# Optimization experiments

Measured on AMD Instinct MI355X. Metric: run time of the kernel, lower is better.

## Reference

```python
import jax, jax.numpy as jnp
import numpy as np

N, M_CTX, SIN, YDIM, SPROJ = 16384, 4096, 256, 7, 256


def setup_inputs() -> dict:
    key = jax.random.key(0)
    k1, k2, k3, k4, k5 = jax.random.split(key, 5)
    return {
        "x": jax.random.normal(k1, (N, SIN), dtype=jnp.float32),
        "y": jax.random.normal(k2, (M_CTX, YDIM), dtype=jnp.float32),
        "Wq": jax.random.normal(k3, (SIN, SPROJ), dtype=jnp.float32) / np.sqrt(SIN),
        "Wk": jax.random.normal(k4, (YDIM, SPROJ), dtype=jnp.float32) / np.sqrt(YDIM),
        "Wv": jax.random.normal(k5, (YDIM, SPROJ), dtype=jnp.float32) / np.sqrt(YDIM),
    }


def smooth_softmax(x):
    # softmax over keys (axis=1) blended with 0.1*relu, renormalized
    s = jax.nn.softmax(x, axis=1)
    num = jax.nn.relu(x) * 0.1 + s
    return num / jnp.sum(num, axis=1, keepdims=True)


def reference(x, y, Wq, Wk, Wv):
    XQ = x @ Wq            # [N, P]
    YK = y @ Wk            # [M, P]
    YV = y @ Wv            # [M, P]
    scores = (XQ @ YK.T) / jnp.sqrt(jnp.asarray(YK.shape[1], XQ.dtype))  # [N, M]
    A = smooth_softmax(scores)
    return A @ YV          # [N, P]
```

## Files before the change

kernel.cpp:

```cpp
#include <hip/hip_runtime.h>
#include <hip/hip_bf16.h>

#define N_Q   16384
#define MCTX  4096
#define DSIN  256
#define YDIM  7
#define PDIM  256
#define BK    32

typedef __attribute__((ext_vector_type(8))) short s16x8;
typedef __attribute__((ext_vector_type(4))) float f32x4;
typedef unsigned short u16;

static __device__ __forceinline__ u16 f2bf(float f) {
    union { float f; unsigned u; } v; v.f = f;
    unsigned r = v.u + 0x7fffu + ((v.u >> 16) & 1u);
    return (u16)(r >> 16);
}
static __device__ __forceinline__ float bf2f(u16 h) {
    union { unsigned u; float f; } v; v.u = ((unsigned)h) << 16;
    return v.f;
}
static __device__ __forceinline__ f32x4 mfma16(s16x8 a, s16x8 b, f32x4 c) {
    return __builtin_amdgcn_mfma_f32_16x16x32_bf16(a, b, c, 0, 0, 0);
}
static __device__ __forceinline__ void gload_lds16(const u16* g, u16* l) {
    __builtin_amdgcn_global_load_lds(
        (const __attribute__((address_space(1))) unsigned int*)(g),
        (__attribute__((address_space(3))) unsigned int*)(l), 16, 0, 0);
}

__global__ void k_wt(const float* __restrict__ Wq, u16* __restrict__ WtH,
                     u16* __restrict__ WtL) {
    int n = blockIdx.x;
    int k = threadIdx.x;
    float w = Wq[(size_t)k * PDIM + n];
    u16 h = f2bf(w);
    WtH[(size_t)n * DSIN + k] = h;
    WtL[(size_t)n * DSIN + k] = f2bf(w - bf2f(h));
}

__global__ void k_ykv(const float* __restrict__ y, const float* __restrict__ Wk,
                      const float* __restrict__ Wv, u16* __restrict__ YK,
                      u16* __restrict__ YVb) {
    int kb = blockIdx.x;
    int p  = threadIdx.x;
    float wk[YDIM], wv[YDIM];
#pragma unroll
    for (int j = 0; j < YDIM; ++j) {
        wk[j] = Wk[(size_t)j * PDIM + p];
        wv[j] = Wv[(size_t)j * PDIM + p];
    }
    u16 vbuf[32];
#pragma unroll
    for (int m = 0; m < 32; ++m) {
        int key = kb * 32 + m;
        float ak = 0.f, av = 0.f;
#pragma unroll
        for (int j = 0; j < YDIM; ++j) {
            float yy = y[(size_t)key * YDIM + j];
            ak += yy * wk[j];
            av += yy * wv[j];
        }
        YK[(size_t)key * PDIM + p] = f2bf(ak * 0.0625f);
        vbuf[m] = f2bf(av);
    }
    s16x8* dst = (s16x8*)(YVb + ((size_t)kb * PDIM + p) * 32);
#pragma unroll
    for (int c = 0; c < 4; ++c) dst[c] = ((s16x8*)vbuf)[c];
}

__global__ __launch_bounds__(256, 1) void k_xq(const float* __restrict__ x,
                                               const u16* __restrict__ WtH,
                                               const u16* __restrict__ WtL,
                                               u16* __restrict__ XQ) {
    __shared__ u16 xH[64 * 256];
    __shared__ u16 xL[64 * 256];
    const int tid = threadIdx.x;
    const int rowg0 = blockIdx.x * 64;

#pragma unroll
    for (int i = 0; i < 8; ++i) {
        int row = (tid >> 5) + i * 8;
        int c32 = tid & 31;
        const float* px = x + (size_t)(rowg0 + row) * DSIN + c32 * 8;
        float4 a = *(const float4*)px;
        float4 b = *(const float4*)(px + 4);
        float vals[8] = {a.x, a.y, a.z, a.w, b.x, b.y, b.z, b.w};
        s16x8 h, l;
#pragma unroll
        for (int j = 0; j < 8; ++j) {
            u16 hh = f2bf(vals[j]);
            h[j] = (short)hh;
            l[j] = (short)f2bf(vals[j] - bf2f(hh));
        }
        int pc = c32 ^ (row & 7);
        *(s16x8*)(xH + row * 256 + pc * 8) = h;
        *(s16x8*)(xL + row * 256 + pc * 8) = l;
    }
    __syncthreads();

    const int wave = tid >> 6, lane = tid & 63;
    const int quad = lane >> 4, m16 = lane & 15;
    const int rowl = wave * 16 + m16;
    const int swz = rowl & 7;
    s16x8 ah[8], al[8];
#pragma unroll
    for (int kf = 0; kf < 8; ++kf) {
        int pc = (kf * 4 + quad) ^ swz;
        ah[kf] = *(const s16x8*)(xH + rowl * 256 + pc * 8);
        al[kf] = *(const s16x8*)(xL + rowl * 256 + pc * 8);
    }
#pragma unroll
    for (int pt = 0; pt < 16; ++pt) {
        f32x4 acc = (f32x4){0.f, 0.f, 0.f, 0.f};
#pragma unroll
        for (int kf = 0; kf < 8; ++kf) {
            size_t idx = (size_t)(pt * 16 + m16) * DSIN + kf * 32 + quad * 8;
            s16x8 bh = *(const s16x8*)(WtH + idx);
            s16x8 bl = *(const s16x8*)(WtL + idx);
            acc = mfma16(ah[kf], bh, acc);
            acc = mfma16(al[kf], bh, acc);
            acc = mfma16(ah[kf], bl, acc);
        }
#pragma unroll
        for (int r = 0; r < 4; ++r)
            XQ[(size_t)(rowg0 + wave * 16 + quad * 4 + r) * PDIM + pt * 16 + m16] =
                f2bf(acc[r]);
    }
}

__global__ __launch_bounds__(256, 2) void k_attn(const u16* __restrict__ XQ,
                                                 const u16* __restrict__ YK,
                                                 const u16* __restrict__ YVb,
                                                 float* __restrict__ accE,
                                                 float* __restrict__ accR,
                                                 float* __restrict__ lsum,
                                                 float* __restrict__ rsum,
                                                 int msPerSplit) {
    __shared__ u16 Kt[32 * 256];
    __shared__ u16 Pe[64 * 40];
    __shared__ u16 Pr[64 * 40];

    const int tid = threadIdx.x;
    const int wave = tid >> 6, lane = tid & 63;
    const int quad = lane >> 4, m16 = lane & 15;
    const int split = blockIdx.y;
    const int qbase = blockIdx.x * 64;
    const int key_begin = split * msPerSplit;
    const int iters = msPerSplit / BK;
    const int pslice = wave * 64;
    const int swz = m16 & 7;

    s16x8 qf[8];
    const u16* qp = XQ + (size_t)(qbase + wave * 16 + m16) * DSIN;
#pragma unroll
    for (int kf = 0; kf < 8; ++kf)
        qf[kf] = *(const s16x8*)(qp + kf * 32 + quad * 8);

    f32x4 aE[4][4], aR[4][4];
#pragma unroll
    for (int g = 0; g < 4; ++g)
#pragma unroll
        for (int t = 0; t < 4; ++t) {
            aE[g][t] = (f32x4){0.f, 0.f, 0.f, 0.f};
            aR[g][t] = (f32x4){0.f, 0.f, 0.f, 0.f};
        }
    float lacc[4] = {0.f, 0.f, 0.f, 0.f}, racc[4] = {0.f, 0.f, 0.f, 0.f};

    auto stage = [&](int key0) {
#pragma unroll
        for (int c = 0; c < 4; ++c) {
            int l = (wave * 4 + c) * 64 + lane;
            int r = l >> 5;
            int sc = (l & 31) ^ (r & 7);
            gload_lds16(YK + (size_t)(key0 + r) * DSIN + sc * 8,
                        Kt + (size_t)(wave * 4 + c) * 512);
        }
    };
    stage(key_begin);

    for (int it = 0; it < iters; ++it) {
        const int key0 = key_begin + it * BK;
        __syncthreads();

        f32x4 s0 = (f32x4){0.f, 0.f, 0.f, 0.f};
        f32x4 s1 = (f32x4){0.f, 0.f, 0.f, 0.f};
#pragma unroll
        for (int kf = 0; kf < 8; ++kf) {
            int pc = (kf * 4 + quad) ^ swz;
            s16x8 b0 = *(const s16x8*)(Kt + m16 * 256 + pc * 8);
            s16x8 b1 = *(const s16x8*)(Kt + (16 + m16) * 256 + pc * 8);
            s0 = mfma16(qf[kf], b0, s0);
            s1 = mfma16(qf[kf], b1, s1);
        }
#pragma unroll
        for (int r = 0; r < 4; ++r) {
            float e0 = __expf(s0[r]), e1 = __expf(s1[r]);
            float rl0 = fmaxf(s0[r], 0.f), rl1 = fmaxf(s1[r], 0.f);
            lacc[r] += e0 + e1;
            racc[r] += rl0 + rl1;
            int row = wave * 16 + quad * 4 + r;
            Pe[row * 40 + m16]      = f2bf(e0);
            Pe[row * 40 + 16 + m16] = f2bf(e1);
            Pr[row * 40 + m16]      = f2bf(rl0);
            Pr[row * 40 + 16 + m16] = f2bf(rl1);
        }
        __syncthreads();

        s16x8 vf[4];
        const u16* vb = YVb + (size_t)((key0 >> 5) * PDIM) * 32;
#pragma unroll
        for (int t = 0; t < 4; ++t)
            vf[t] = *(const s16x8*)(vb + (size_t)(pslice + t * 16 + m16) * 32 + quad * 8);

        if (it + 1 < iters) stage(key0 + BK);

#pragma unroll
        for (int g = 0; g < 4; ++g) {
            s16x8 pa = *(const s16x8*)(Pe + (g * 16 + m16) * 40 + quad * 8);
            s16x8 pb = *(const s16x8*)(Pr + (g * 16 + m16) * 40 + quad * 8);
#pragma unroll
            for (int t = 0; t < 4; ++t) {
                aE[g][t] = mfma16(pa, vf[t], aE[g][t]);
                aR[g][t] = mfma16(pb, vf[t], aR[g][t]);
            }
        }
    }

    size_t ob = ((size_t)split * N_Q + qbase) * PDIM;
#pragma unroll
    for (int g = 0; g < 4; ++g)
#pragma unroll
        for (int t = 0; t < 4; ++t)
#pragma unroll
            for (int r = 0; r < 4; ++r) {
                size_t o = ob + (size_t)(g * 16 + quad * 4 + r) * PDIM + pslice + t * 16 + m16;
                accE[o] = aE[g][t][r];
                accR[o] = aR[g][t][r];
            }
#pragma unroll
    for (int r = 0; r < 4; ++r) {
        lacc[r] += __shfl_xor(lacc[r], 1);
        lacc[r] += __shfl_xor(lacc[r], 2);
        lacc[r] += __shfl_xor(lacc[r], 4);
        lacc[r] += __shfl_xor(lacc[r], 8);
        racc[r] += __shfl_xor(racc[r], 1);
        racc[r] += __shfl_xor(racc[r], 2);
        racc[r] += __shfl_xor(racc[r], 4);
        racc[r] += __shfl_xor(racc[r], 8);
    }
    if (m16 < 4) {
        float lv = (m16 == 0) ? lacc[0] : (m16 == 1) ? lacc[1] : (m16 == 2) ? lacc[2] : lacc[3];
        float rv = (m16 == 0) ? racc[0] : (m16 == 1) ? racc[1] : (m16 == 2) ? racc[2] : racc[3];
        int row = split * N_Q + qbase + wave * 16 + quad * 4 + m16;
        lsum[row] = lv;
        rsum[row] = rv;
    }
}

__global__ void k_comb(const float* __restrict__ accE, const float* __restrict__ accR,
                       const float* __restrict__ lsum, const float* __restrict__ rsum,
                       float* __restrict__ out, int nsplit) {
    int row = blockIdx.x * 4 + (threadIdx.x >> 6);
    size_t idx = (size_t)row * PDIM + (threadIdx.x & 63) * 4;
    const size_t NP = (size_t)N_Q * PDIM;
    float4 E = {0.f, 0.f, 0.f, 0.f}, R = {0.f, 0.f, 0.f, 0.f};
    float L = 0.f, Rs = 0.f;
    for (int s = 0; s < nsplit; ++s) {
        float4 e = *(const float4*)(accE + s * NP + idx);
        float4 r = *(const float4*)(accR + s * NP + idx);
        E.x += e.x; E.y += e.y; E.z += e.z; E.w += e.w;
        R.x += r.x; R.y += r.y; R.z += r.z; R.w += r.w;
        L  += lsum[(size_t)s * N_Q + row];
        Rs += rsum[(size_t)s * N_Q + row];
    }
    float invL = 1.f / L, invD = 1.f / (1.f + 0.1f * Rs);
    float4 o;
    o.x = (0.1f * R.x + E.x * invL) * invD;
    o.y = (0.1f * R.y + E.y * invL) * invD;
    o.z = (0.1f * R.z + E.z * invL) * invD;
    o.w = (0.1f * R.w + E.w * invL) * invD;
    *(float4*)(out + idx) = o;
}

extern "C" void kernel_launch(void* const* d_in, const int* in_sizes, int n_in,
                              void* d_out, int out_size, void* d_ws, size_t ws_size,
                              hipStream_t stream) {
    const float* x  = (const float*)d_in[0];
    const float* y  = (const float*)d_in[1];
    const float* Wq = (const float*)d_in[2];
    const float* Wk = (const float*)d_in[3];
    const float* Wv = (const float*)d_in[4];
    float* out = (float*)d_out;

    char* ws = (char*)d_ws;
    size_t off = 0;
    auto take = [&](size_t bytes) -> char* {
        char* p = ws + off;
        off += (bytes + 255) & ~(size_t)255;
        return p;
    };
    u16* XQ  = (u16*)take((size_t)N_Q * PDIM * 2);
    u16* WtH = (u16*)take((size_t)PDIM * DSIN * 2);
    u16* WtL = (u16*)take((size_t)PDIM * DSIN * 2);
    u16* YK  = (u16*)take((size_t)MCTX * PDIM * 2);
    u16* YVb = (u16*)take((size_t)MCTX * PDIM * 2);

    size_t perSplit = (size_t)N_Q * PDIM * 4 * 2 + (size_t)N_Q * 4 * 2 + 1024;
    int nsplit = (ws_size >= off + 2 * perSplit + 4096) ? 2 : 1;

    float* accE = (float*)take((size_t)nsplit * N_Q * PDIM * 4);
    float* accR = (float*)take((size_t)nsplit * N_Q * PDIM * 4);
    float* lsum = (float*)take((size_t)nsplit * N_Q * 4);
    float* rsum = (float*)take((size_t)nsplit * N_Q * 4);

    hipLaunchKernelGGL(k_wt,   dim3(PDIM),     dim3(DSIN), 0, stream, Wq, WtH, WtL);
    hipLaunchKernelGGL(k_ykv,  dim3(MCTX/32),  dim3(PDIM), 0, stream, y, Wk, Wv, YK, YVb);
    hipLaunchKernelGGL(k_xq,   dim3(N_Q/64),   dim3(256),  0, stream, x, WtH, WtL, XQ);
    hipLaunchKernelGGL(k_attn, dim3(N_Q/64, nsplit), dim3(256), 0, stream,
                       XQ, YK, YVb, accE, accR, lsum, rsum, MCTX / nsplit);
    hipLaunchKernelGGL(k_comb, dim3(N_Q/4),    dim3(256),  0, stream,
                       accE, accR, lsum, rsum, out, nsplit);
}
```

Before: 236.3 us.

## Split keys four ways, store partials in bf16, retile projection kernels

The attention kernel now writes its per-split partial accumulators as bf16 instead of fp32. That halves the workspace traffic for the partials, and the saved space lets the launcher pick four key splits when the workspace is large enough, so more blocks run at once. k_xq is retiled to 32 rows per block with waves splitting the output columns, for higher occupancy. k_ykv uses 1024 threads with an interleaved key order in YVb that matches the new packed 32-bit P stores in LDS. k_comb reads 8 bf16 values per thread. Rounding the partial sums to bf16 before combining adds accuracy risk.

```diff
diff --git a/kernel.cpp b/kernel.cpp
--- a/kernel.cpp
+++ b/kernel.cpp
@@ -7,6 +7,7 @@
 #define YDIM  7
 #define PDIM  256
 #define BK    32
+#define PSTR  40
 
 typedef __attribute__((ext_vector_type(8))) short s16x8;
 typedef __attribute__((ext_vector_type(4))) float f32x4;
@@ -44,16 +45,19 @@
                       const float* __restrict__ Wv, u16* __restrict__ YK,
                       u16* __restrict__ YVb) {
     int kb = blockIdx.x;
-    int p  = threadIdx.x;
+    int p  = threadIdx.x & 255;
+    int quarter = threadIdx.x >> 8;
     float wk[YDIM], wv[YDIM];
 #pragma unroll
     for (int j = 0; j < YDIM; ++j) {
         wk[j] = Wk[(size_t)j * PDIM + p];
         wv[j] = Wv[(size_t)j * PDIM + p];
     }
-    u16 vbuf[32];
-#pragma unroll
-    for (int m = 0; m < 32; ++m) {
+    s16x8 vbuf;
+#pragma unroll
+    for (int i = 0; i < 8; ++i) {
+        int slot = quarter * 8 + i;
+        int m = (slot & 1) * 16 + (slot >> 1);
         int key = kb * 32 + m;
         float ak = 0.f, av = 0.f;
 #pragma unroll
@@ -63,26 +67,24 @@
             av += yy * wv[j];
         }
         YK[(size_t)key * PDIM + p] = f2bf(ak * 0.0625f);
-        vbuf[m] = f2bf(av);
-    }
-    s16x8* dst = (s16x8*)(YVb + ((size_t)kb * PDIM + p) * 32);
-#pragma unroll
-    for (int c = 0; c < 4; ++c) dst[c] = ((s16x8*)vbuf)[c];
-}
-
-__global__ __launch_bounds__(256, 1) void k_xq(const float* __restrict__ x,
+        vbuf[i] = (short)f2bf(av);
+    }
+    *(s16x8*)(YVb + ((size_t)kb * PDIM + p) * 32 + quarter * 8) = vbuf;
+}
+
+__global__ __launch_bounds__(256, 4) void k_xq(const float* __restrict__ x,
                                                const u16* __restrict__ WtH,
                                                const u16* __restrict__ WtL,
                                                u16* __restrict__ XQ) {
-    __shared__ u16 xH[64 * 256];
-    __shared__ u16 xL[64 * 256];
+    __shared__ u16 xH[32 * 256];
+    __shared__ u16 xL[32 * 256];
     const int tid = threadIdx.x;
-    const int rowg0 = blockIdx.x * 64;
-
-#pragma unroll
-    for (int i = 0; i < 8; ++i) {
-        int row = (tid >> 5) + i * 8;
-        int c32 = tid & 31;
+    const int rowg0 = blockIdx.x * 32;
+
+#pragma unroll
+    for (int i = 0; i < 4; ++i) {
+        int idx = i * 256 + tid;
+        int row = idx >> 5, c32 = idx & 31;
         const float* px = x + (size_t)(rowg0 + row) * DSIN + c32 * 8;
         float4 a = *(const float4*)px;
         float4 b = *(const float4*)(px + 4);
@@ -102,7 +104,9 @@
 
     const int wave = tid >> 6, lane = tid & 63;
     const int quad = lane >> 4, m16 = lane & 15;
-    const int rowl = wave * 16 + m16;
+    const int mtile = wave >> 1;
+    const int phalf = (wave & 1) * 8;
+    const int rowl = mtile * 16 + m16;
     const int swz = rowl & 7;
     s16x8 ah[8], al[8];
 #pragma unroll
@@ -112,11 +116,12 @@
         al[kf] = *(const s16x8*)(xL + rowl * 256 + pc * 8);
     }
 #pragma unroll
-    for (int pt = 0; pt < 16; ++pt) {
+    for (int pt = 0; pt < 8; ++pt) {
+        int ptg = phalf + pt;
         f32x4 acc = (f32x4){0.f, 0.f, 0.f, 0.f};
 #pragma unroll
         for (int kf = 0; kf < 8; ++kf) {
-            size_t idx = (size_t)(pt * 16 + m16) * DSIN + kf * 32 + quad * 8;
+            size_t idx = (size_t)(ptg * 16 + m16) * DSIN + kf * 32 + quad * 8;
             s16x8 bh = *(const s16x8*)(WtH + idx);
             s16x8 bl = *(const s16x8*)(WtL + idx);
             acc = mfma16(ah[kf], bh, acc);
@@ -125,7 +130,7 @@
         }
 #pragma unroll
         for (int r = 0; r < 4; ++r)
-            XQ[(size_t)(rowg0 + wave * 16 + quad * 4 + r) * PDIM + pt * 16 + m16] =
+            XQ[(size_t)(rowg0 + mtile * 16 + quad * 4 + r) * PDIM + ptg * 16 + m16] =
                 f2bf(acc[r]);
     }
 }
@@ -133,14 +138,14 @@
 __global__ __launch_bounds__(256, 2) void k_attn(const u16* __restrict__ XQ,
                                                  const u16* __restrict__ YK,
                                                  const u16* __restrict__ YVb,
-                                                 float* __restrict__ accE,
-                                                 float* __restrict__ accR,
+                                                 u16* __restrict__ accE,
+                                                 u16* __restrict__ accR,
                                                  float* __restrict__ lsum,
                                                  float* __restrict__ rsum,
                                                  int msPerSplit) {
     __shared__ u16 Kt[32 * 256];
-    __shared__ u16 Pe[64 * 40];
-    __shared__ u16 Pr[64 * 40];
+    __shared__ u16 Pe[64 * PSTR];
+    __shared__ u16 Pr[64 * PSTR];
 
     const int tid = threadIdx.x;
     const int wave = tid >> 6, lane = tid & 63;
@@ -201,10 +206,10 @@
             lacc[r] += e0 + e1;
             racc[r] += rl0 + rl1;
             int row = wave * 16 + quad * 4 + r;
-            Pe[row * 40 + m16]      = f2bf(e0);
-            Pe[row * 40 + 16 + m16] = f2bf(e1);
-            Pr[row * 40 + m16]      = f2bf(rl0);
-            Pr[row * 40 + 16 + m16] = f2bf(rl1);
+            unsigned pe = (unsigned)f2bf(e0) | ((unsigned)f2bf(e1) << 16);
+            unsigned pr = (unsigned)f2bf(rl0) | ((unsigned)f2bf(rl1) << 16);
+            *(unsigned*)(&Pe[row * PSTR + 2 * m16]) = pe;
+            *(unsigned*)(&Pr[row * PSTR + 2 * m16]) = pr;
         }
         __syncthreads();
 
@@ -218,8 +223,8 @@
 
 #pragma unroll
         for (int g = 0; g < 4; ++g) {
-            s16x8 pa = *(const s16x8*)(Pe + (g * 16 + m16) * 40 + quad * 8);
-            s16x8 pb = *(const s16x8*)(Pr + (g * 16 + m16) * 40 + quad * 8);
+            s16x8 pa = *(const s16x8*)(&Pe[(g * 16 + m16) * PSTR + quad * 8]);
+            s16x8 pb = *(const s16x8*)(&Pr[(g * 16 + m16) * PSTR + quad * 8]);
 #pragma unroll
             for (int t = 0; t < 4; ++t) {
                 aE[g][t] = mfma16(pa, vf[t], aE[g][t]);
@@ -236,8 +241,8 @@
 #pragma unroll
             for (int r = 0; r < 4; ++r) {
                 size_t o = ob + (size_t)(g * 16 + quad * 4 + r) * PDIM + pslice + t * 16 + m16;
-                accE[o] = aE[g][t][r];
-                accR[o] = aR[g][t][r];
+                accE[o] = f2bf(aE[g][t][r]);
+                accR[o] = f2bf(aR[g][t][r]);
             }
 #pragma unroll
     for (int r = 0; r < 4; ++r) {
@@ -259,29 +264,40 @@
     }
 }
 
-__global__ void k_comb(const float* __restrict__ accE, const float* __restrict__ accR,
+__global__ void k_comb(const u16* __restrict__ accE, const u16* __restrict__ accR,
                        const float* __restrict__ lsum, const float* __restrict__ rsum,
                        float* __restrict__ out, int nsplit) {
-    int row = blockIdx.x * 4 + (threadIdx.x >> 6);
-    size_t idx = (size_t)row * PDIM + (threadIdx.x & 63) * 4;
+    size_t chunk = (size_t)blockIdx.x * 256 + threadIdx.x;
+    int row = (int)(chunk >> 5);
+    size_t base = (size_t)row * PDIM + (chunk & 31) * 8;
     const size_t NP = (size_t)N_Q * PDIM;
-    float4 E = {0.f, 0.f, 0.f, 0.f}, R = {0.f, 0.f, 0.f, 0.f};
+    float E[8], R[8];
+#pragma unroll
+    for (int j = 0; j < 8; ++j) { E[j] = 0.f; R[j] = 0.f; }
     float L = 0.f, Rs = 0.f;
     for (int s = 0; s < nsplit; ++s) {
-        float4 e = *(const float4*)(accE + s * NP + idx);
-        float4 r = *(const float4*)(accR + s * NP + idx);
-        E.x += e.x; E.y += e.y; E.z += e.z; E.w += e.w;
-        R.x += r.x; R.y += r.y; R.z += r.z; R.w += r.w;
+        s16x8 e = *(const s16x8*)(accE + s * NP + base);
+        s16x8 r = *(const s16x8*)(accR + s * NP + base);
+#pragma unroll
+        for (int j = 0; j < 8; ++j) {
+            E[j] += bf2f((u16)e[j]);
+            R[j] += bf2f((u16)r[j]);
+        }
         L  += lsum[(size_t)s * N_Q + row];
         Rs += rsum[(size_t)s * N_Q + row];
     }
     float invL = 1.f / L, invD = 1.f / (1.f + 0.1f * Rs);
-    float4 o;
-    o.x = (0.1f * R.x + E.x * invL) * invD;
-    o.y = (0.1f * R.y + E.y * invL) * invD;
-    o.z = (0.1f * R.z + E.z * invL) * invD;
-    o.w = (0.1f * R.w + E.w * invL) * invD;
-    *(float4*)(out + idx) = o;
+    float4 o0, o1;
+    o0.x = (0.1f * R[0] + E[0] * invL) * invD;
+    o0.y = (0.1f * R[1] + E[1] * invL) * invD;
+    o0.z = (0.1f * R[2] + E[2] * invL) * invD;
+    o0.w = (0.1f * R[3] + E[3] * invL) * invD;
+    o1.x = (0.1f * R[4] + E[4] * invL) * invD;
+    o1.y = (0.1f * R[5] + E[5] * invL) * invD;
+    o1.z = (0.1f * R[6] + E[6] * invL) * invD;
+    o1.w = (0.1f * R[7] + E[7] * invL) * invD;
+    *(float4*)(out + base) = o0;
+    *(float4*)(out + base + 4) = o1;
 }
 
 extern "C" void kernel_launch(void* const* d_in, const int* in_sizes, int n_in,
@@ -307,19 +323,21 @@
     u16* YK  = (u16*)take((size_t)MCTX * PDIM * 2);
     u16* YVb = (u16*)take((size_t)MCTX * PDIM * 2);
 
-    size_t perSplit = (size_t)N_Q * PDIM * 4 * 2 + (size_t)N_Q * 4 * 2 + 1024;
-    int nsplit = (ws_size >= off + 2 * perSplit + 4096) ? 2 : 1;
-
-    float* accE = (float*)take((size_t)nsplit * N_Q * PDIM * 4);
-    float* accR = (float*)take((size_t)nsplit * N_Q * PDIM * 4);
+    size_t perSplit = (size_t)N_Q * PDIM * 2 * 2 + (size_t)N_Q * 4 * 2 + 1024;
+    int nsplit = 1;
+    if (ws_size >= off + 4 * perSplit + 4096) nsplit = 4;
+    else if (ws_size >= off + 2 * perSplit + 4096) nsplit = 2;
+
+    u16*   accE = (u16*)take((size_t)nsplit * N_Q * PDIM * 2);
+    u16*   accR = (u16*)take((size_t)nsplit * N_Q * PDIM * 2);
     float* lsum = (float*)take((size_t)nsplit * N_Q * 4);
     float* rsum = (float*)take((size_t)nsplit * N_Q * 4);
 
     hipLaunchKernelGGL(k_wt,   dim3(PDIM),     dim3(DSIN), 0, stream, Wq, WtH, WtL);
-    hipLaunchKernelGGL(k_ykv,  dim3(MCTX/32),  dim3(PDIM), 0, stream, y, Wk, Wv, YK, YVb);
-    hipLaunchKernelGGL(k_xq,   dim3(N_Q/64),   dim3(256),  0, stream, x, WtH, WtL, XQ);
+    hipLaunchKernelGGL(k_ykv,  dim3(MCTX/32),  dim3(1024), 0, stream, y, Wk, Wv, YK, YVb);
+    hipLaunchKernelGGL(k_xq,   dim3(N_Q/32),   dim3(256),  0, stream, x, WtH, WtL, XQ);
     hipLaunchKernelGGL(k_attn, dim3(N_Q/64, nsplit), dim3(256), 0, stream,
                        XQ, YK, YVb, accE, accR, lsum, rsum, MCTX / nsplit);
-    hipLaunchKernelGGL(k_comb, dim3(N_Q/4),    dim3(256),  0, stream,
+    hipLaunchKernelGGL(k_comb, dim3((N_Q * PDIM) / (256 * 8)), dim3(256), 0, stream,
                        accE, accR, lsum, rsum, out, nsplit);
 }
```

After: 239.6 us. Within noise of the previous version (+1.4%).
